# Kernel tuning notes

Hardware: AMD Instinct MI355X
Metric: run time of the kernel (lower is better)

The kernel has to match this reference:

```python
import jax, jax.numpy as jnp
import numpy as np

EDGE_WEIGHT = 2.0
NUM_CLASSES = 3

def _cross_shifts(x, pad_val):
    # x: [B,H,W]; returns list of 5 cross-neighborhood views (center,up,down,left,right)
    p = jnp.pad(x, ((0, 0), (1, 1), (1, 1)), constant_values=pad_val)
    return [p[:, 1:-1, 1:-1], p[:, :-2, 1:-1], p[:, 2:, 1:-1],
            p[:, 1:-1, :-2], p[:, 1:-1, 2:]]

def boundary_mask(targets):
    # cv2 MORPH_ELLIPSE (3,3) == 4-connected cross; dilate=max-filter, erode=min-filter.
    # cv2 morphology default border: -inf for dilate, +inf for erode (emulated with 0 / 255).
    t = targets.astype(jnp.int32)
    shifts_d = _cross_shifts(t, 0)
    shifts_e = _cross_shifts(t, 255)
    dilated = shifts_d[0]
    eroded = shifts_e[0]
    for d, e in zip(shifts_d[1:], shifts_e[1:]):
        dilated = jnp.maximum(dilated, d)
        eroded = jnp.minimum(eroded, e)
    # cv2 computes uint8 bitwise xor of dilated ^ eroded
    return jnp.bitwise_xor(dilated.astype(jnp.uint8), eroded.astype(jnp.uint8))

def setup_inputs() -> dict:
    key = jax.random.key(0)
    k1, k2 = jax.random.split(key)
    predictions = jax.random.normal(k1, (32, NUM_CLASSES, 512, 512), dtype=jnp.float32)
    targets = jax.random.randint(k2, (32, 512, 512), 0, NUM_CLASSES).astype(jnp.int64)
    return {"predictions": predictions, "targets": targets}

def reference(predictions, targets):
    edge_map = boundary_mask(targets).astype(predictions.dtype)  # [B,H,W]
    logp = jax.nn.log_softmax(predictions, axis=1)               # [B,C,H,W]
    ce = -jnp.take_along_axis(logp, targets[:, None, :, :].astype(jnp.int32), axis=1)[:, 0]  # [B,H,W]
    weighted = ce * (1.0 + EDGE_WEIGHT * edge_map)
    return weighted.mean()
```

## Files before the change

### kernel.cpp

```cpp
#include <hip/hip_runtime.h>

#define BB 32
#define HH 512
#define WW 512

constexpr int PLANE = HH * WW;
constexpr long long NPIX = (long long)BB * HH * WW;
constexpr int BLOCK = 256;
constexpr int GRID = (BB * HH) / 4;

__global__ __launch_bounds__(256) void edge_loss_kernel(
    const float* __restrict__ pred,
    const int* __restrict__ tgt,
    double* __restrict__ partial)
{
    const int lane = threadIdx.x & 63;
    const int wid  = threadIdx.x >> 6;
    const int row  = blockIdx.x * 4 + wid;
    const int h    = row & (HH - 1);
    const int b    = row >> 9;

    const int rbase = row * WW;
    const int wA = 4 * lane;
    const int wB = 256 + 4 * lane;

    const int4 cA4 = *reinterpret_cast<const int4*>(tgt + rbase + wA);
    const int4 cB4 = *reinterpret_cast<const int4*>(tgt + rbase + wB);
    const int cA[4] = { cA4.x, cA4.y, cA4.z, cA4.w };
    const int cB[4] = { cB4.x, cB4.y, cB4.z, cB4.w };

    const bool hasu = (h > 0);
    const bool hasd = (h < HH - 1);
    int uA[4], uB[4], dA[4], dB[4];
    if (hasu) {
        const int4 a = *reinterpret_cast<const int4*>(tgt + rbase - WW + wA);
        const int4 bb = *reinterpret_cast<const int4*>(tgt + rbase - WW + wB);
        uA[0]=a.x; uA[1]=a.y; uA[2]=a.z; uA[3]=a.w;
        uB[0]=bb.x; uB[1]=bb.y; uB[2]=bb.z; uB[3]=bb.w;
    }
    if (hasd) {
        const int4 a = *reinterpret_cast<const int4*>(tgt + rbase + WW + wA);
        const int4 bb = *reinterpret_cast<const int4*>(tgt + rbase + WW + wB);
        dA[0]=a.x; dA[1]=a.y; dA[2]=a.z; dA[3]=a.w;
        dB[0]=bb.x; dB[1]=bb.y; dB[2]=bb.z; dB[3]=bb.w;
    }

    const int lA = __shfl_up(cA[3], 1, 64);
    const int lB = __shfl_up(cB[3], 1, 64);
    const int rA = __shfl_down(cA[0], 1, 64);
    const int rB = __shfl_down(cB[0], 1, 64);
    const int a3_63 = __shfl(cA[3], 63, 64);
    const int b0_0  = __shfl(cB[0], 0, 64);

    const int leftA_d  = (lane == 0)  ? 0      : lA;
    const int leftA_e  = (lane == 0)  ? 255    : lA;
    const int leftB_v  = (lane == 0)  ? a3_63  : lB;
    const int rightA_v = (lane == 63) ? b0_0   : rA;
    const int rightB_d = (lane == 63) ? 0      : rB;
    const int rightB_e = (lane == 63) ? 255    : rB;

    const float* pp = pred + (size_t)(b * 3) * PLANE + (size_t)h * WW;
    const float4 pA0 = *reinterpret_cast<const float4*>(pp + wA);
    const float4 pB0 = *reinterpret_cast<const float4*>(pp + wB);
    const float4 pA1 = *reinterpret_cast<const float4*>(pp + PLANE + wA);
    const float4 pB1 = *reinterpret_cast<const float4*>(pp + PLANE + wB);
    const float4 pA2 = *reinterpret_cast<const float4*>(pp + 2 * PLANE + wA);
    const float4 pB2 = *reinterpret_cast<const float4*>(pp + 2 * PLANE + wB);

    const float L2E = 1.4426950408889634f;
    const float LN2 = 0.6931471805599453f;
    float sum = 0.0f;

    auto proc4 = [&](const int c[4], const int u[4], const int d[4],
                     int ld, int le, int rd, int re,
                     const float4& P0, const float4& P1, const float4& P2) {
        const float C0[4] = { P0.x, P0.y, P0.z, P0.w };
        const float C1[4] = { P1.x, P1.y, P1.z, P1.w };
        const float C2[4] = { P2.x, P2.y, P2.z, P2.w };
        #pragma unroll
        for (int i = 0; i < 4; ++i) {
            const int lv_d = (i == 0) ? ld : c[i - 1];
            const int lv_e = (i == 0) ? le : c[i - 1];
            const int rv_d = (i == 3) ? rd : c[i + 1];
            const int rv_e = (i == 3) ? re : c[i + 1];
            int dil = max(c[i], max(lv_d, rv_d));
            int ero = min(c[i], min(lv_e, rv_e));
            if (hasu) { dil = max(dil, u[i]); ero = min(ero, u[i]); }
            if (hasd) { dil = max(dil, d[i]); ero = min(ero, d[i]); }
            const int edge = dil ^ ero;

            const float pa = C0[i], pb = C1[i], pc = C2[i];
            const float s = __builtin_amdgcn_exp2f(pa * L2E)
                          + __builtin_amdgcn_exp2f(pb * L2E)
                          + __builtin_amdgcn_exp2f(pc * L2E);
            const float lse = LN2 * __builtin_amdgcn_logf(s);
            const float pt  = (c[i] == 0) ? pa : ((c[i] == 1) ? pb : pc);
            const float wgt = fmaf(2.0f, (float)edge, 1.0f);
            sum = fmaf(lse - pt, wgt, sum);
        }
    };

    proc4(cA, uA, dA, leftA_d, leftA_e, rightA_v, rightA_v, pA0, pA1, pA2);
    proc4(cB, uB, dB, leftB_v, leftB_v, rightB_d, rightB_e, pB0, pB1, pB2);

    #pragma unroll
    for (int off = 32; off; off >>= 1)
        sum += __shfl_down(sum, off, 64);

    __shared__ float wsum[4];
    if (lane == 0) wsum[wid] = sum;
    __syncthreads();
    if (threadIdx.x == 0)
        partial[blockIdx.x] = (double)(wsum[0] + wsum[1] + wsum[2] + wsum[3]);
}

__global__ __launch_bounds__(256) void finalize_kernel(
    const double* __restrict__ partial, float* __restrict__ out)
{
    double s = 0.0;
    #pragma unroll
    for (int i = 0; i < GRID / 256; ++i)
        s += partial[i * 256 + threadIdx.x];
    #pragma unroll
    for (int off = 32; off; off >>= 1)
        s += __shfl_down(s, off, 64);
    __shared__ double wsum[4];
    const int lane = threadIdx.x & 63;
    if (lane == 0) wsum[threadIdx.x >> 6] = s;
    __syncthreads();
    if (threadIdx.x == 0)
        out[0] = (float)((wsum[0] + wsum[1] + wsum[2] + wsum[3]) / (double)NPIX);
}

extern "C" void kernel_launch(void* const* d_in, const int* in_sizes, int n_in,
                              void* d_out, int out_size, void* d_ws, size_t ws_size,
                              hipStream_t stream) {
    const float* pred = (const float*)d_in[0];
    const int*   tgt  = (const int*)d_in[1];
    double* partial = (double*)d_ws;
    float*  out     = (float*)d_out;

    edge_loss_kernel<<<GRID, BLOCK, 0, stream>>>(pred, tgt, partial);
    finalize_kernel<<<1, BLOCK, 0, stream>>>(partial, out);
}
```

Baseline: 29.10 us.

## Process two rows per wave to reuse target rows and drop block reduction

Each wavefront now handles two adjacent image rows, so the shared middle target rows serve as both center and vertical neighbor. Target loads per row drop from three to two, and more predictions loads are in flight per thread. The per-block shared-memory reduction and syncthreads are removed; each wave writes a float partial, and the finalize kernel reads them with float4 loads. The grid is halved and register pressure rises, which may reduce latency hiding.

```diff
diff --git a/kernel.cpp b/kernel.cpp
--- a/kernel.cpp
+++ b/kernel.cpp
@@ -7,86 +7,85 @@
 constexpr int PLANE = HH * WW;
 constexpr long long NPIX = (long long)BB * HH * WW;
 constexpr int BLOCK = 256;
-constexpr int GRID = (BB * HH) / 4;
+constexpr int NWAVES = BB * HH / 2;
+constexpr int GRID = NWAVES / 4;
 
 __global__ __launch_bounds__(256) void edge_loss_kernel(
     const float* __restrict__ pred,
     const int* __restrict__ tgt,
-    double* __restrict__ partial)
+    float* __restrict__ partial)
 {
     const int lane = threadIdx.x & 63;
     const int wid  = threadIdx.x >> 6;
-    const int row  = blockIdx.x * 4 + wid;
-    const int h    = row & (HH - 1);
-    const int b    = row >> 9;
+    const int gw   = blockIdx.x * 4 + wid;
+    const int r0   = gw * 2;
+    const int h0   = r0 & (HH - 1);
+    const int b    = r0 >> 9;
 
-    const int rbase = row * WW;
     const int wA = 4 * lane;
     const int wB = 256 + 4 * lane;
+    const int base0 = r0 * WW;
 
-    const int4 cA4 = *reinterpret_cast<const int4*>(tgt + rbase + wA);
-    const int4 cB4 = *reinterpret_cast<const int4*>(tgt + rbase + wB);
-    const int cA[4] = { cA4.x, cA4.y, cA4.z, cA4.w };
-    const int cB[4] = { cB4.x, cB4.y, cB4.z, cB4.w };
+    const int4 t0A4 = *reinterpret_cast<const int4*>(tgt + base0 + wA);
+    const int4 t0B4 = *reinterpret_cast<const int4*>(tgt + base0 + wB);
+    const int4 t1A4 = *reinterpret_cast<const int4*>(tgt + base0 + WW + wA);
+    const int4 t1B4 = *reinterpret_cast<const int4*>(tgt + base0 + WW + wB);
+    const int t0A[4] = { t0A4.x, t0A4.y, t0A4.z, t0A4.w };
+    const int t0B[4] = { t0B4.x, t0B4.y, t0B4.z, t0B4.w };
+    const int t1A[4] = { t1A4.x, t1A4.y, t1A4.z, t1A4.w };
+    const int t1B[4] = { t1B4.x, t1B4.y, t1B4.z, t1B4.w };
 
-    const bool hasu = (h > 0);
-    const bool hasd = (h < HH - 1);
-    int uA[4], uB[4], dA[4], dB[4];
+    const bool hasu = (h0 > 0);
+    const bool hasd = (h0 < HH - 2);
+    int tmA[4], tmB[4], t2A[4], t2B[4];
     if (hasu) {
-        const int4 a = *reinterpret_cast<const int4*>(tgt + rbase - WW + wA);
-        const int4 bb = *reinterpret_cast<const int4*>(tgt + rbase - WW + wB);
-        uA[0]=a.x; uA[1]=a.y; uA[2]=a.z; uA[3]=a.w;
-        uB[0]=bb.x; uB[1]=bb.y; uB[2]=bb.z; uB[3]=bb.w;
+        const int4 a = *reinterpret_cast<const int4*>(tgt + base0 - WW + wA);
+        const int4 bb = *reinterpret_cast<const int4*>(tgt + base0 - WW + wB);
+        tmA[0]=a.x; tmA[1]=a.y; tmA[2]=a.z; tmA[3]=a.w;
+        tmB[0]=bb.x; tmB[1]=bb.y; tmB[2]=bb.z; tmB[3]=bb.w;
     }
     if (hasd) {
-        const int4 a = *reinterpret_cast<const int4*>(tgt + rbase + WW + wA);
-        const int4 bb = *reinterpret_cast<const int4*>(tgt + rbase + WW + wB);
-        dA[0]=a.x; dA[1]=a.y; dA[2]=a.z; dA[3]=a.w;
-        dB[0]=bb.x; dB[1]=bb.y; dB[2]=bb.z; dB[3]=bb.w;
+        const int4 a = *reinterpret_cast<const int4*>(tgt + base0 + 2 * WW + wA);
+        const int4 bb = *reinterpret_cast<const int4*>(tgt + base0 + 2 * WW + wB);
+        t2A[0]=a.x; t2A[1]=a.y; t2A[2]=a.z; t2A[3]=a.w;
+        t2B[0]=bb.x; t2B[1]=bb.y; t2B[2]=bb.z; t2B[3]=bb.w;
     }
 
-    const int lA = __shfl_up(cA[3], 1, 64);
-    const int lB = __shfl_up(cB[3], 1, 64);
-    const int rA = __shfl_down(cA[0], 1, 64);
-    const int rB = __shfl_down(cB[0], 1, 64);
-    const int a3_63 = __shfl(cA[3], 63, 64);
-    const int b0_0  = __shfl(cB[0], 0, 64);
-
-    const int leftA_d  = (lane == 0)  ? 0      : lA;
-    const int leftA_e  = (lane == 0)  ? 255    : lA;
-    const int leftB_v  = (lane == 0)  ? a3_63  : lB;
-    const int rightA_v = (lane == 63) ? b0_0   : rA;
-    const int rightB_d = (lane == 63) ? 0      : rB;
-    const int rightB_e = (lane == 63) ? 255    : rB;
-
-    const float* pp = pred + (size_t)(b * 3) * PLANE + (size_t)h * WW;
-    const float4 pA0 = *reinterpret_cast<const float4*>(pp + wA);
-    const float4 pB0 = *reinterpret_cast<const float4*>(pp + wB);
-    const float4 pA1 = *reinterpret_cast<const float4*>(pp + PLANE + wA);
-    const float4 pB1 = *reinterpret_cast<const float4*>(pp + PLANE + wB);
-    const float4 pA2 = *reinterpret_cast<const float4*>(pp + 2 * PLANE + wA);
-    const float4 pB2 = *reinterpret_cast<const float4*>(pp + 2 * PLANE + wB);
+    const float* pp0 = pred + (size_t)(b * 3) * PLANE + (size_t)h0 * WW;
+    const float4 p0A0 = *reinterpret_cast<const float4*>(pp0 + wA);
+    const float4 p0B0 = *reinterpret_cast<const float4*>(pp0 + wB);
+    const float4 p0A1 = *reinterpret_cast<const float4*>(pp0 + PLANE + wA);
+    const float4 p0B1 = *reinterpret_cast<const float4*>(pp0 + PLANE + wB);
+    const float4 p0A2 = *reinterpret_cast<const float4*>(pp0 + 2 * PLANE + wA);
+    const float4 p0B2 = *reinterpret_cast<const float4*>(pp0 + 2 * PLANE + wB);
+    const float4 p1A0 = *reinterpret_cast<const float4*>(pp0 + WW + wA);
+    const float4 p1B0 = *reinterpret_cast<const float4*>(pp0 + WW + wB);
+    const float4 p1A1 = *reinterpret_cast<const float4*>(pp0 + WW + PLANE + wA);
+    const float4 p1B1 = *reinterpret_cast<const float4*>(pp0 + WW + PLANE + wB);
+    const float4 p1A2 = *reinterpret_cast<const float4*>(pp0 + WW + 2 * PLANE + wA);
+    const float4 p1B2 = *reinterpret_cast<const float4*>(pp0 + WW + 2 * PLANE + wB);
 
     const float L2E = 1.4426950408889634f;
     const float LN2 = 0.6931471805599453f;
     float sum = 0.0f;
 
-    auto proc4 = [&](const int c[4], const int u[4], const int d[4],
-                     int ld, int le, int rd, int re,
+    auto proc4 = [&](const int c[4], const int* u, const int* d,
+                     bool has_up, bool has_down,
+                     int ld_, int le_, int rd_, int re_,
                      const float4& P0, const float4& P1, const float4& P2) {
         const float C0[4] = { P0.x, P0.y, P0.z, P0.w };
         const float C1[4] = { P1.x, P1.y, P1.z, P1.w };
         const float C2[4] = { P2.x, P2.y, P2.z, P2.w };
         #pragma unroll
         for (int i = 0; i < 4; ++i) {
-            const int lv_d = (i == 0) ? ld : c[i - 1];
-            const int lv_e = (i == 0) ? le : c[i - 1];
-            const int rv_d = (i == 3) ? rd : c[i + 1];
-            const int rv_e = (i == 3) ? re : c[i + 1];
+            const int lv_d = (i == 0) ? ld_ : c[i - 1];
+            const int lv_e = (i == 0) ? le_ : c[i - 1];
+            const int rv_d = (i == 3) ? rd_ : c[i + 1];
+            const int rv_e = (i == 3) ? re_ : c[i + 1];
             int dil = max(c[i], max(lv_d, rv_d));
             int ero = min(c[i], min(lv_e, rv_e));
-            if (hasu) { dil = max(dil, u[i]); ero = min(ero, u[i]); }
-            if (hasd) { dil = max(dil, d[i]); ero = min(ero, d[i]); }
+            if (has_up)   { dil = max(dil, u[i]); ero = min(ero, u[i]); }
+            if (has_down) { dil = max(dil, d[i]); ero = min(ero, d[i]); }
             const int edge = dil ^ ero;
 
             const float pa = C0[i], pb = C1[i], pc = C2[i];
@@ -100,27 +99,47 @@
         }
     };
 
-    proc4(cA, uA, dA, leftA_d, leftA_e, rightA_v, rightA_v, pA0, pA1, pA2);
-    proc4(cB, uB, dB, leftB_v, leftB_v, rightB_d, rightB_e, pB0, pB1, pB2);
+    auto procrow = [&](const int cA[4], const int cB[4],
+                       const int* uA, const int* uB, const int* dA, const int* dB,
+                       bool has_up, bool has_down,
+                       const float4& PA0, const float4& PA1, const float4& PA2,
+                       const float4& PB0, const float4& PB1, const float4& PB2) {
+        const int lA = __shfl_up(cA[3], 1, 64);
+        const int lB = __shfl_up(cB[3], 1, 64);
+        const int rA = __shfl_down(cA[0], 1, 64);
+        const int rB = __shfl_down(cB[0], 1, 64);
+        const int a3_63 = __shfl(cA[3], 63, 64);
+        const int b0_0  = __shfl(cB[0], 0, 64);
+        const int leftA_d  = (lane == 0)  ? 0     : lA;
+        const int leftA_e  = (lane == 0)  ? 255   : lA;
+        const int leftB_v  = (lane == 0)  ? a3_63 : lB;
+        const int rightA_v = (lane == 63) ? b0_0  : rA;
+        const int rightB_d = (lane == 63) ? 0     : rB;
+        const int rightB_e = (lane == 63) ? 255   : rB;
+        proc4(cA, uA, dA, has_up, has_down, leftA_d, leftA_e, rightA_v, rightA_v, PA0, PA1, PA2);
+        proc4(cB, uB, dB, has_up, has_down, leftB_v, leftB_v, rightB_d, rightB_e, PB0, PB1, PB2);
+    };
+
+    procrow(t0A, t0B, tmA, tmB, t1A, t1B, hasu, true,
+            p0A0, p0A1, p0A2, p0B0, p0B1, p0B2);
+    procrow(t1A, t1B, t0A, t0B, t2A, t2B, true, hasd,
+            p1A0, p1A1, p1A2, p1B0, p1B1, p1B2);
 
     #pragma unroll
     for (int off = 32; off; off >>= 1)
         sum += __shfl_down(sum, off, 64);
-
-    __shared__ float wsum[4];
-    if (lane == 0) wsum[wid] = sum;
-    __syncthreads();
-    if (threadIdx.x == 0)
-        partial[blockIdx.x] = (double)(wsum[0] + wsum[1] + wsum[2] + wsum[3]);
+    if (lane == 0) partial[gw] = sum;
 }
 
 __global__ __launch_bounds__(256) void finalize_kernel(
-    const double* __restrict__ partial, float* __restrict__ out)
+    const float* __restrict__ partial, float* __restrict__ out)
 {
     double s = 0.0;
     #pragma unroll
-    for (int i = 0; i < GRID / 256; ++i)
-        s += partial[i * 256 + threadIdx.x];
+    for (int i = 0; i < NWAVES / (256 * 4); ++i) {
+        const float4 v = *reinterpret_cast<const float4*>(partial + i * 1024 + threadIdx.x * 4);
+        s += (double)v.x + (double)v.y + (double)v.z + (double)v.w;
+    }
     #pragma unroll
     for (int off = 32; off; off >>= 1)
         s += __shfl_down(s, off, 64);
@@ -137,8 +156,8 @@
                               hipStream_t stream) {
     const float* pred = (const float*)d_in[0];
     const int*   tgt  = (const int*)d_in[1];
-    double* partial = (double*)d_ws;
-    float*  out     = (float*)d_out;
+    float* partial = (float*)d_ws;
+    float* out     = (float*)d_out;
 
     edge_loss_kernel<<<GRID, BLOCK, 0, stream>>>(pred, tgt, partial);
     finalize_kernel<<<1, BLOCK, 0, stream>>>(partial, out);
```

Result: faster. 28.24 us (-2.9%).
